# Kernel tuning notes

Hardware: AMD Instinct MI355X
Metric: run time of the kernel (lower is better)

Reference implementation:

```python
import jax, jax.numpy as jnp
import numpy as np

KERNEL = 5
STRIDE = 1
DN = ('NHWC', 'HWIO', 'NHWC')
PRIOR_VAR = 0.01


def setup_inputs() -> dict:
    key = jax.random.key(0)
    k1, k2, k3 = jax.random.split(key, 3)
    mu_in = jax.random.normal(k1, (32, 224, 224, 3), dtype=jnp.float32)
    # GlorotNormal-ish scale for a 5x5x3 -> 64 kernel
    w_mu = jax.random.normal(k2, (5, 5, 3, 64), dtype=jnp.float32) * 0.12
    # original init: uniform in [min_sigma, ini_sigma] = [-4.6, -2.25]
    w_sigma = jax.random.uniform(k3, (64,), dtype=jnp.float32, minval=-4.6, maxval=-2.25)
    return {"mu_in": mu_in, "w_mu": w_mu, "w_sigma": w_sigma}


def reference(mu_in, w_mu, w_sigma):
    # KL regularizer: broadcast of (64,) logvar against (5,5,3,64) mu, mean over all
    kl = 0.5 * jnp.mean(
        jnp.log(PRIOR_VAR) - 1.0 - w_sigma
        + jax.nn.softplus(w_sigma) / PRIOR_VAR
        + jnp.square(w_mu) / PRIOR_VAR
    )

    w_sigma_2 = jax.nn.softplus(w_sigma)  # log(1+exp(w_sigma))

    # Mean path: standard conv2d, VALID, stride 1, NHWC
    mu_out = jax.lax.conv_general_dilated(
        mu_in, w_mu, (STRIDE, STRIDE), 'VALID', dimension_numbers=DN
    )  # [B, Ho, Wo, K]

    # Variance path: per-output-location sum over the k*k*C patch of x^2 / x_dim.
    # Same math as the original extract_patches + reduce_sum, but computed as a
    # channel-summed box filter on x^2 (no im2col materialization).
    C = mu_in.shape[-1]
    x_dim = jnp.asarray(KERNEL * KERNEL * C, mu_in.dtype)
    ones_k = jnp.ones((KERNEL, KERNEL, C, 1), mu_in.dtype)
    sq = jax.lax.conv_general_dilated(
        jnp.square(mu_in), ones_k, (STRIDE, STRIDE), 'VALID', dimension_numbers=DN
    ) / x_dim  # [B, Ho, Wo, 1]

    Sigma_out = jax.nn.softplus(w_sigma_2 * sq)  # broadcast -> [B, Ho, Wo, K]
    return (mu_out, Sigma_out, kl)
```

## Files before the change

### kernel.cpp

```cpp
#include <hip/hip_runtime.h>
#include <math.h>

#define BATCH 32
#define HIN   224
#define WIN   224
#define CIN   3
#define KOUT  64
#define RK    5
#define HOUT  220
#define WOUT  220

#define TS       16
#define PATCH    20
#define NT_TILES (14 * 14 * BATCH)
#define NBLK     1024
#define NTOT ((size_t)BATCH * HOUT * WOUT * KOUT)

typedef float  v4f    __attribute__((ext_vector_type(4)));
typedef short  short8 __attribute__((ext_vector_type(8)));

#define WS_WF_FRAGS 768
#define WS_WSG_OFF  12288
#define WS_CNT_OFF  12544

__device__ __forceinline__ float exp2_hw(float x) { float r; asm("v_exp_f32 %0, %1" : "=v"(r) : "v"(x)); return r; }
__device__ __forceinline__ float log2_hw(float x) { float r; asm("v_log_f32 %0, %1" : "=v"(r) : "v"(x)); return r; }
#define LOG2E 1.44269504088896f
#define LN2   0.69314718055995f

__device__ __forceinline__ float softplus_hw(float x) {
    float t = exp2_hw(-fabsf(x) * LOG2E);
    return fmaxf(x, 0.0f) + LN2 * log2_hw(1.0f + t);
}
__device__ __forceinline__ float softplus_pos(float y) {
    return y + LN2 * log2_hw(1.0f + exp2_hw(-y * LOG2E));
}
__device__ __forceinline__ short f2bf(float x) {
    unsigned u = __float_as_uint(x);
    u = (u + 0x7FFFu + ((u >> 16) & 1u)) >> 16;
    return (short)u;
}

__global__ __launch_bounds__(256) void vdp_prep_kernel(
    const float* __restrict__ w_mu, const float* __restrict__ w_sigma,
    void* __restrict__ ws, float* __restrict__ out)
{
    __shared__ float red[4];
    short8* wf = (short8*)ws;
    float* wsg = (float*)((char*)ws + WS_WSG_OFF);
    const int t = threadIdx.x;

    if (t == 0) *(int*)((char*)ws + WS_CNT_OFF) = NBLK;

    for (int f = t; f < WS_WF_FRAGS; f += 256) {
        const int s  = f >> 8;
        const int nb = (f >> 6) & 3;
        const int l  = f & 63;
        const int ch = nb * 16 + (l & 15);
        const int h2 = l >> 4;
        short8 r;
        #pragma unroll
        for (int i = 0; i < 8; ++i) {
            const int k = s * 32 + h2 * 8 + i;
            const int kh = k >> 4, inner = k & 15;
            float v = 0.0f;
            if (inner < 15 && k < 80) {
                const int kw = inner / 3;
                const int c  = inner - kw * 3;
                v = w_mu[((kh * 5 + kw) * 3 + c) * KOUT + ch];
            }
            r[i] = f2bf(v);
        }
        wf[f] = r;
    }
    if (t < KOUT) wsg[t] = softplus_hw(w_sigma[t]);

    float s = 0.0f;
    for (int i = t; i < RK * RK * CIN * KOUT; i += 256) {
        const float v = w_mu[i];
        s = fmaf(v, v, s);
    }
    float u = s * (100.0f / 4800.0f);
    if (t < KOUT) {
        const float wsv = w_sigma[t];
        u += (-wsv + softplus_hw(wsv) * 100.0f) * (1.0f / 64.0f);
    }
    #pragma unroll
    for (int off = 32; off > 0; off >>= 1)
        u += __shfl_down(u, off, 64);
    if ((t & 63) == 0) red[t >> 6] = u;
    __syncthreads();
    if (t == 0) {
        const float U = red[0] + red[1] + red[2] + red[3];
        out[2 * NTOT] = 0.5f * (-4.6051701860f - 1.0f + U);
    }
}

__device__ __forceinline__ void stage_tile(const float* __restrict__ mu_in, int t,
                                           float* buf, int tid)
{
    const int b  = t / 196;
    const int r2 = t - b * 196;
    int ho0 = (r2 / 14) * TS; if (ho0 > HOUT - TS) ho0 = HOUT - TS;
    int wo0 = (r2 % 14) * TS; if (wo0 > WOUT - TS) wo0 = WOUT - TS;
    const float* gb = mu_in + ((size_t)b * HIN + ho0) * (WIN * CIN) + wo0 * CIN;
    #pragma unroll
    for (int it = 0; it < 2; ++it) {
        const int ci = it * 256 + (tid & ~63);
        if (ci < 320) {
            const int il = ci + (tid & 63);
            const int r  = il >> 4;
            int cc = il & 15; if (cc > 14) cc = 14;
            const float* g = gb + r * (WIN * CIN) + cc * 4;
            __builtin_amdgcn_global_load_lds(
                (const __attribute__((address_space(1))) void*)g,
                (__attribute__((address_space(3))) void*)(buf + ci * 4),
                16, 0, 0);
        }
    }
}

__global__ __launch_bounds__(256, 4) void vdp_conv_kernel(
    const float* __restrict__ mu_in, void* __restrict__ ws, float* __restrict__ out)
{
    __shared__ float s_row[2][PATCH * 64];
    __shared__ float s_ssq[PATCH][PATCH];
    __shared__ float s_sq[TS * TS];
    __shared__ int   s_next;

    const int tid  = threadIdx.x;
    const int lane = tid & 63;
    const int wid  = tid >> 6;
    const int p    = lane & 15;
    const int h2   = lane >> 4;

    int* cnt = (int*)((char*)ws + WS_CNT_OFF);

    const short8* wfg = (const short8*)ws;
    short8 wf[12];
    #pragma unroll
    for (int f = 0; f < 12; ++f) wf[f] = wfg[f * 64 + lane];
    const float* wsg_g = (const float*)((const char*)ws + WS_WSG_OFF);
    const v4f wsg_kg = *(const v4f*)(wsg_g + p * 4);

    int t = blockIdx.x;
    int cur = 0;
    stage_tile(mu_in, t, s_row[0], tid);
    asm volatile("s_waitcnt vmcnt(0)" ::: "memory");

    while (t < NT_TILES) {
        asm volatile("s_waitcnt vmcnt(24) lgkmcnt(0)" ::: "memory");
        __builtin_amdgcn_s_barrier();
        __builtin_amdgcn_sched_barrier(0);

        const float* srow = s_row[cur];

        if (tid == 0) s_next = atomicAdd(cnt, 1);

        for (int idx = tid; idx < PATCH * PATCH; idx += 256) {
            const int r = idx / PATCH;
            const int px = idx - r * PATCH;
            const float x0 = srow[r * 64 + 3 * px], x1 = srow[r * 64 + 3 * px + 1],
                        x2 = srow[r * 64 + 3 * px + 2];
            s_ssq[r][px] = fmaf(x0, x0, fmaf(x1, x1, x2 * x2));
        }
        asm volatile("s_waitcnt lgkmcnt(0)" ::: "memory");
        __builtin_amdgcn_s_barrier();

        {
            const int pr = tid >> 4, pc = tid & 15;
            float acc = 0.0f;
            #pragma unroll
            for (int kh = 0; kh < RK; ++kh)
                #pragma unroll
                for (int kw = 0; kw < RK; ++kw)
                    acc += s_ssq[pr + kh][pc + kw];
            s_sq[tid] = acc * (1.0f / 75.0f);
        }
        asm volatile("s_waitcnt lgkmcnt(0)" ::: "memory");
        __builtin_amdgcn_s_barrier();

        const int tn = s_next;
        if (tn < NT_TILES) stage_tile(mu_in, tn, s_row[cur ^ 1], tid);
        __builtin_amdgcn_sched_barrier(0);

        const int b  = t / 196;
        const int r2 = t - b * 196;
        int ho0 = (r2 / 14) * TS; if (ho0 > HOUT - TS) ho0 = HOUT - TS;
        int wo0 = (r2 % 14) * TS; if (wo0 > WOUT - TS) wo0 = WOUT - TS;

        #pragma unroll 1
        for (int j = 0; j < 4; ++j) {
            const int rt = (wid << 2) | j;
            const size_t rowbase = (((size_t)b * HOUT + ho0 + rt) * WOUT + wo0) * KOUT;

            short8 pf[3];
            #pragma unroll
            for (int s = 0; s < 3; ++s) {
                int ridx = rt + 2 * s + (h2 >> 1);
                ridx = ridx > PATCH - 1 ? PATCH - 1 : ridx;
                const float* rp = srow + ridx * 64 + 3 * p + 8 * (h2 & 1);
                union { unsigned u[4]; short8 v; } cv;
                asm("v_cvt_pk_bf16_f32 %0, %1, %2" : "=v"(cv.u[0]) : "v"(rp[0]), "v"(rp[1]));
                asm("v_cvt_pk_bf16_f32 %0, %1, %2" : "=v"(cv.u[1]) : "v"(rp[2]), "v"(rp[3]));
                asm("v_cvt_pk_bf16_f32 %0, %1, %2" : "=v"(cv.u[2]) : "v"(rp[4]), "v"(rp[5]));
                asm("v_cvt_pk_bf16_f32 %0, %1, %2" : "=v"(cv.u[3]) : "v"(rp[6]), "v"(rp[7]));
                pf[s] = cv.v;
            }

            v4f acc[4];
            #pragma unroll
            for (int nb = 0; nb < 4; ++nb) {
                v4f a = {0.0f, 0.0f, 0.0f, 0.0f};
                #pragma unroll
                for (int s = 0; s < 3; ++s)
                    a = __builtin_amdgcn_mfma_f32_16x16x32_bf16(wf[s * 4 + nb], pf[s], a, 0, 0, 0);
                acc[nb] = a;
            }

            float* mp = out + rowbase + (size_t)p * KOUT + h2 * 4;
            #pragma unroll
            for (int nb = 0; nb < 4; ++nb)
                *(v4f*)(mp + nb * 16) = acc[nb];

            float* sp = out + NTOT + rowbase + p * 4;
            #pragma unroll
            for (int pp = 0; pp < 4; ++pp) {
                const int px = (h2 << 2) | pp;
                const float sq = s_sq[(rt << 4) | px];
                v4f sg;
                sg.x = softplus_pos(wsg_kg.x * sq);
                sg.y = softplus_pos(wsg_kg.y * sq);
                sg.z = softplus_pos(wsg_kg.z * sq);
                sg.w = softplus_pos(wsg_kg.w * sq);
                *(v4f*)(sp + (size_t)px * KOUT) = sg;
            }
        }

        t = tn;
        cur ^= 1;
    }
}

extern "C" void kernel_launch(void* const* d_in, const int* in_sizes, int n_in,
                              void* d_out, int out_size, void* d_ws, size_t ws_size,
                              hipStream_t stream)
{
    (void)in_sizes; (void)n_in; (void)ws_size; (void)out_size;
    const float* mu_in   = (const float*)d_in[0];
    const float* w_mu    = (const float*)d_in[1];
    const float* w_sigma = (const float*)d_in[2];
    float* out = (float*)d_out;

    vdp_prep_kernel<<<1, 256, 0, stream>>>(w_mu, w_sigma, d_ws, out);
    vdp_conv_kernel<<<NBLK, 256, 0, stream>>>(mu_in, d_ws, out);
}
```

Baseline: 186.5 us.

## Replace 16x16 tiles with full-width two-row strips and separable box filter

Each block now processes four consecutive full-width strips of two output rows each. Blocks are assigned statically with an XCD-aware block remap, replacing the atomic work-stealing counter. Each strip stages six contiguous input rows into LDS with double buffering. The variance box filter is computed separably, with column sums first and a horizontal 5-tap sum at output time. The aim is contiguous global loads and row-contiguous output writes, plus removal of the atomic scheduling overhead. The costs are roughly twice as much staged input per output pixel and a much larger LDS footprint, which could pressure occupancy.

```diff
diff --git a/kernel.cpp b/kernel.cpp
--- a/kernel.cpp
+++ b/kernel.cpp
@@ -10,10 +10,12 @@
 #define HOUT  220
 #define WOUT  220
 
-#define TS       16
-#define PATCH    20
-#define NT_TILES (14 * 14 * BATCH)
-#define NBLK     1024
+#define STRIPS_Y  110
+#define NSTRIP    (STRIPS_Y * BATCH)
+#define NBLK      880
+#define ROWF      (WIN * CIN)
+#define SROW_FL   (6 * ROWF)
+#define SROW_CH   (SROW_FL / 4)
 #define NTOT ((size_t)BATCH * HOUT * WOUT * KOUT)
 
 typedef float  v4f    __attribute__((ext_vector_type(4)));
@@ -21,7 +23,6 @@
 
 #define WS_WF_FRAGS 768
 #define WS_WSG_OFF  12288
-#define WS_CNT_OFF  12544
 
 __device__ __forceinline__ float exp2_hw(float x) { float r; asm("v_exp_f32 %0, %1" : "=v"(r) : "v"(x)); return r; }
 __device__ __forceinline__ float log2_hw(float x) { float r; asm("v_log_f32 %0, %1" : "=v"(r) : "v"(x)); return r; }
@@ -49,8 +50,6 @@
     short8* wf = (short8*)ws;
     float* wsg = (float*)((char*)ws + WS_WSG_OFF);
     const int t = threadIdx.x;
-
-    if (t == 0) *(int*)((char*)ws + WS_CNT_OFF) = NBLK;
 
     for (int f = t; f < WS_WF_FRAGS; f += 256) {
         const int s  = f >> 8;
@@ -96,45 +95,45 @@
     }
 }
 
-__device__ __forceinline__ void stage_tile(const float* __restrict__ mu_in, int t,
-                                           float* buf, int tid)
-{
-    const int b  = t / 196;
-    const int r2 = t - b * 196;
-    int ho0 = (r2 / 14) * TS; if (ho0 > HOUT - TS) ho0 = HOUT - TS;
-    int wo0 = (r2 % 14) * TS; if (wo0 > WOUT - TS) wo0 = WOUT - TS;
-    const float* gb = mu_in + ((size_t)b * HIN + ho0) * (WIN * CIN) + wo0 * CIN;
+__device__ __forceinline__ void stage_strip(const float* __restrict__ mu_in, int t,
+                                            float* buf, int tid)
+{
+    const int b  = t / STRIPS_Y;
+    const int sy = t - b * STRIPS_Y;
+    const float* gb = mu_in + ((size_t)b * HIN + sy * 2) * ROWF;
     #pragma unroll
-    for (int it = 0; it < 2; ++it) {
+    for (int it = 0; it < 4; ++it) {
         const int ci = it * 256 + (tid & ~63);
-        if (ci < 320) {
+        if (ci < SROW_CH) {
             const int il = ci + (tid & 63);
-            const int r  = il >> 4;
-            int cc = il & 15; if (cc > 14) cc = 14;
-            const float* g = gb + r * (WIN * CIN) + cc * 4;
-            __builtin_amdgcn_global_load_lds(
-                (const __attribute__((address_space(1))) void*)g,
-                (__attribute__((address_space(3))) void*)(buf + ci * 4),
-                16, 0, 0);
+            if (il < SROW_CH) {
+                __builtin_amdgcn_global_load_lds(
+                    (const __attribute__((address_space(1))) void*)(gb + il * 4),
+                    (__attribute__((address_space(3))) void*)(buf + ci * 4),
+                    16, 0, 0);
+            }
         }
     }
 }
 
 __global__ __launch_bounds__(256, 4) void vdp_conv_kernel(
-    const float* __restrict__ mu_in, void* __restrict__ ws, float* __restrict__ out)
-{
-    __shared__ float s_row[2][PATCH * 64];
-    __shared__ float s_ssq[PATCH][PATCH];
-    __shared__ float s_sq[TS * TS];
-    __shared__ int   s_next;
+    const float* __restrict__ mu_in, const void* __restrict__ ws, float* __restrict__ out)
+{
+    __shared__ float s_row[2][SROW_FL];
+    __shared__ float s_ssq[6][224];
+    __shared__ float s_cs[2][224];
 
     const int tid  = threadIdx.x;
     const int lane = tid & 63;
     const int wid  = tid >> 6;
     const int p    = lane & 15;
     const int h2   = lane >> 4;
-
-    int* cnt = (int*)((char*)ws + WS_CNT_OFF);
+    const int rt   = wid & 1;
+    const int half = wid >> 1;
+
+    const int bid = blockIdx.x;
+    const int wg  = (bid & 7) * (NBLK / 8) + (bid >> 3);
+    const int t0  = wg * 4;
 
     const short8* wfg = (const short8*)ws;
     short8 wf[12];
@@ -143,63 +142,59 @@
     const float* wsg_g = (const float*)((const char*)ws + WS_WSG_OFF);
     const v4f wsg_kg = *(const v4f*)(wsg_g + p * 4);
 
-    int t = blockIdx.x;
+    stage_strip(mu_in, t0, s_row[0], tid);
+    __syncthreads();
+
     int cur = 0;
-    stage_tile(mu_in, t, s_row[0], tid);
-    asm volatile("s_waitcnt vmcnt(0)" ::: "memory");
-
-    while (t < NT_TILES) {
-        asm volatile("s_waitcnt vmcnt(24) lgkmcnt(0)" ::: "memory");
-        __builtin_amdgcn_s_barrier();
+    #pragma unroll 1
+    for (int k4 = 0; k4 < 4; ++k4) {
+        const int t  = t0 + k4;
+        const int b  = t / STRIPS_Y;
+        const int sy = t - b * STRIPS_Y;
+        const int r0 = sy * 2;
+
+        if (k4 < 3) stage_strip(mu_in, t + 1, s_row[cur ^ 1], tid);
         __builtin_amdgcn_sched_barrier(0);
 
         const float* srow = s_row[cur];
 
-        if (tid == 0) s_next = atomicAdd(cnt, 1);
-
-        for (int idx = tid; idx < PATCH * PATCH; idx += 256) {
-            const int r = idx / PATCH;
-            const int px = idx - r * PATCH;
-            const float x0 = srow[r * 64 + 3 * px], x1 = srow[r * 64 + 3 * px + 1],
-                        x2 = srow[r * 64 + 3 * px + 2];
-            s_ssq[r][px] = fmaf(x0, x0, fmaf(x1, x1, x2 * x2));
+        #pragma unroll
+        for (int i = 0; i < 6; ++i) {
+            const int idx = i * 256 + tid;
+            if (idx < 6 * 224) {
+                const int r = idx / 224, px = idx - r * 224;
+                const float* q = srow + r * ROWF + 3 * px;
+                s_ssq[r][px] = fmaf(q[0], q[0], fmaf(q[1], q[1], q[2] * q[2]));
+            }
         }
         asm volatile("s_waitcnt lgkmcnt(0)" ::: "memory");
         __builtin_amdgcn_s_barrier();
 
-        {
-            const int pr = tid >> 4, pc = tid & 15;
-            float acc = 0.0f;
-            #pragma unroll
-            for (int kh = 0; kh < RK; ++kh)
-                #pragma unroll
-                for (int kw = 0; kw < RK; ++kw)
-                    acc += s_ssq[pr + kh][pc + kw];
-            s_sq[tid] = acc * (1.0f / 75.0f);
+        #pragma unroll
+        for (int i = 0; i < 2; ++i) {
+            const int idx = i * 256 + tid;
+            if (idx < 2 * 224) {
+                const int rr = idx / 224, px = idx - rr * 224;
+                s_cs[rr][px] = s_ssq[rr][px] + s_ssq[rr + 1][px] + s_ssq[rr + 2][px]
+                             + s_ssq[rr + 3][px] + s_ssq[rr + 4][px];
+            }
         }
         asm volatile("s_waitcnt lgkmcnt(0)" ::: "memory");
         __builtin_amdgcn_s_barrier();
 
-        const int tn = s_next;
-        if (tn < NT_TILES) stage_tile(mu_in, tn, s_row[cur ^ 1], tid);
-        __builtin_amdgcn_sched_barrier(0);
-
-        const int b  = t / 196;
-        const int r2 = t - b * 196;
-        int ho0 = (r2 / 14) * TS; if (ho0 > HOUT - TS) ho0 = HOUT - TS;
-        int wo0 = (r2 % 14) * TS; if (wo0 > WOUT - TS) wo0 = WOUT - TS;
+        const size_t rowbase = ((size_t)b * HOUT + r0 + rt) * WOUT * KOUT;
 
         #pragma unroll 1
-        for (int j = 0; j < 4; ++j) {
-            const int rt = (wid << 2) | j;
-            const size_t rowbase = (((size_t)b * HOUT + ho0 + rt) * WOUT + wo0) * KOUT;
+        for (int g = 0; g < 7; ++g) {
+            int wo = half ? 112 + 16 * g : 16 * g;
+            if (wo > WOUT - 16) wo = WOUT - 16;
 
             short8 pf[3];
             #pragma unroll
             for (int s = 0; s < 3; ++s) {
                 int ridx = rt + 2 * s + (h2 >> 1);
-                ridx = ridx > PATCH - 1 ? PATCH - 1 : ridx;
-                const float* rp = srow + ridx * 64 + 3 * p + 8 * (h2 & 1);
+                ridx = ridx > 5 ? 5 : ridx;
+                const float* rp = srow + ridx * ROWF + 3 * (wo + p) + 8 * (h2 & 1);
                 union { unsigned u[4]; short8 v; } cv;
                 asm("v_cvt_pk_bf16_f32 %0, %1, %2" : "=v"(cv.u[0]) : "v"(rp[0]), "v"(rp[1]));
                 asm("v_cvt_pk_bf16_f32 %0, %1, %2" : "=v"(cv.u[1]) : "v"(rp[2]), "v"(rp[3]));
@@ -207,7 +202,6 @@
                 asm("v_cvt_pk_bf16_f32 %0, %1, %2" : "=v"(cv.u[3]) : "v"(rp[6]), "v"(rp[7]));
                 pf[s] = cv.v;
             }
-
             v4f acc[4];
             #pragma unroll
             for (int nb = 0; nb < 4; ++nb) {
@@ -217,17 +211,21 @@
                     a = __builtin_amdgcn_mfma_f32_16x16x32_bf16(wf[s * 4 + nb], pf[s], a, 0, 0, 0);
                 acc[nb] = a;
             }
-
-            float* mp = out + rowbase + (size_t)p * KOUT + h2 * 4;
+            float* mp = out + rowbase + (size_t)(wo + p) * KOUT + h2 * 4;
             #pragma unroll
             for (int nb = 0; nb < 4; ++nb)
                 *(v4f*)(mp + nb * 16) = acc[nb];
-
+        }
+
+        {
+            const int px0 = half * 112;
+            const int nq  = half ? 27 : 28;
             float* sp = out + NTOT + rowbase + p * 4;
-            #pragma unroll
-            for (int pp = 0; pp < 4; ++pp) {
-                const int px = (h2 << 2) | pp;
-                const float sq = s_sq[(rt << 4) | px];
+            #pragma unroll 1
+            for (int q = 0; q < nq; ++q) {
+                const int px = px0 + ((q << 2) | h2);
+                const float sq = (s_cs[rt][px] + s_cs[rt][px + 1] + s_cs[rt][px + 2]
+                                + s_cs[rt][px + 3] + s_cs[rt][px + 4]) * (1.0f / 75.0f);
                 v4f sg;
                 sg.x = softplus_pos(wsg_kg.x * sq);
                 sg.y = softplus_pos(wsg_kg.y * sq);
@@ -237,7 +235,8 @@
             }
         }
 
-        t = tn;
+        asm volatile("s_waitcnt vmcnt(48) lgkmcnt(0)" ::: "memory");
+        __builtin_amdgcn_s_barrier();
         cur ^= 1;
     }
 }
```

After: 196.4 us. 1.05x slower.

## Replace persistent atomic tile scheduler with one-block-per-tile grid launch

Applied to the files above, without the earlier changes.

Drops the persistent-kernel design, with its atomic work counter and double-buffered LDS prefetch of the next tile, in favour of a 3D grid where each block handles exactly one 16x16 output tile. The variance box-filter sum moves out of a separate LDS pass: it is computed per row in registers and broadcast with wave shuffles, so the s_sq buffer and one barrier disappear. The prep kernel is also spread over four blocks. The launch now has about six thousand blocks instead of 1024 persistent ones, which loses the overlap of tile loading with compute but removes the atomic and the loop overhead. Each block also reloads the weight fragments, which the persistent version loaded only once per block.

```diff
diff --git a/kernel.cpp b/kernel.cpp
--- a/kernel.cpp
+++ b/kernel.cpp
@@ -12,8 +12,6 @@
 
 #define TS       16
 #define PATCH    20
-#define NT_TILES (14 * 14 * BATCH)
-#define NBLK     1024
 #define NTOT ((size_t)BATCH * HOUT * WOUT * KOUT)
 
 typedef float  v4f    __attribute__((ext_vector_type(4)));
@@ -21,7 +19,6 @@
 
 #define WS_WF_FRAGS 768
 #define WS_WSG_OFF  12288
-#define WS_CNT_OFF  12544
 
 __device__ __forceinline__ float exp2_hw(float x) { float r; asm("v_exp_f32 %0, %1" : "=v"(r) : "v"(x)); return r; }
 __device__ __forceinline__ float log2_hw(float x) { float r; asm("v_log_f32 %0, %1" : "=v"(r) : "v"(x)); return r; }
@@ -49,10 +46,10 @@
     short8* wf = (short8*)ws;
     float* wsg = (float*)((char*)ws + WS_WSG_OFF);
     const int t = threadIdx.x;
-
-    if (t == 0) *(int*)((char*)ws + WS_CNT_OFF) = NBLK;
-
-    for (int f = t; f < WS_WF_FRAGS; f += 256) {
+    const int blk = blockIdx.x;
+
+    if (blk < 3) {
+        const int f = blk * 256 + t;
         const int s  = f >> 8;
         const int nb = (f >> 6) & 3;
         const int l  = f & 63;
@@ -72,7 +69,9 @@
             r[i] = f2bf(v);
         }
         wf[f] = r;
-    }
+        return;
+    }
+
     if (t < KOUT) wsg[t] = softplus_hw(w_sigma[t]);
 
     float s = 0.0f;
@@ -96,37 +95,11 @@
     }
 }
 
-__device__ __forceinline__ void stage_tile(const float* __restrict__ mu_in, int t,
-                                           float* buf, int tid)
+__global__ __launch_bounds__(256, 4) void vdp_conv_kernel(
+    const float* __restrict__ mu_in, const void* __restrict__ ws, float* __restrict__ out)
 {
-    const int b  = t / 196;
-    const int r2 = t - b * 196;
-    int ho0 = (r2 / 14) * TS; if (ho0 > HOUT - TS) ho0 = HOUT - TS;
-    int wo0 = (r2 % 14) * TS; if (wo0 > WOUT - TS) wo0 = WOUT - TS;
-    const float* gb = mu_in + ((size_t)b * HIN + ho0) * (WIN * CIN) + wo0 * CIN;
-    #pragma unroll
-    for (int it = 0; it < 2; ++it) {
-        const int ci = it * 256 + (tid & ~63);
-        if (ci < 320) {
-            const int il = ci + (tid & 63);
-            const int r  = il >> 4;
-            int cc = il & 15; if (cc > 14) cc = 14;
-            const float* g = gb + r * (WIN * CIN) + cc * 4;
-            __builtin_amdgcn_global_load_lds(
-                (const __attribute__((address_space(1))) void*)g,
-                (__attribute__((address_space(3))) void*)(buf + ci * 4),
-                16, 0, 0);
-        }
-    }
-}
-
-__global__ __launch_bounds__(256, 4) void vdp_conv_kernel(
-    const float* __restrict__ mu_in, void* __restrict__ ws, float* __restrict__ out)
-{
-    __shared__ float s_row[2][PATCH * 64];
+    __shared__ float s_row[PATCH * 64];
     __shared__ float s_ssq[PATCH][PATCH];
-    __shared__ float s_sq[TS * TS];
-    __shared__ int   s_next;
 
     const int tid  = threadIdx.x;
     const int lane = tid & 63;
@@ -134,7 +107,9 @@
     const int p    = lane & 15;
     const int h2   = lane >> 4;
 
-    int* cnt = (int*)((char*)ws + WS_CNT_OFF);
+    const int b = blockIdx.z;
+    int ho0 = blockIdx.y * TS; if (ho0 > HOUT - TS) ho0 = HOUT - TS;
+    int wo0 = blockIdx.x * TS; if (wo0 > WOUT - TS) wo0 = WOUT - TS;
 
     const short8* wfg = (const short8*)ws;
     short8 wf[12];
@@ -143,102 +118,91 @@
     const float* wsg_g = (const float*)((const char*)ws + WS_WSG_OFF);
     const v4f wsg_kg = *(const v4f*)(wsg_g + p * 4);
 
-    int t = blockIdx.x;
-    int cur = 0;
-    stage_tile(mu_in, t, s_row[0], tid);
-    asm volatile("s_waitcnt vmcnt(0)" ::: "memory");
-
-    while (t < NT_TILES) {
-        asm volatile("s_waitcnt vmcnt(24) lgkmcnt(0)" ::: "memory");
-        __builtin_amdgcn_s_barrier();
-        __builtin_amdgcn_sched_barrier(0);
-
-        const float* srow = s_row[cur];
-
-        if (tid == 0) s_next = atomicAdd(cnt, 1);
-
-        for (int idx = tid; idx < PATCH * PATCH; idx += 256) {
-            const int r = idx / PATCH;
-            const int px = idx - r * PATCH;
-            const float x0 = srow[r * 64 + 3 * px], x1 = srow[r * 64 + 3 * px + 1],
-                        x2 = srow[r * 64 + 3 * px + 2];
-            s_ssq[r][px] = fmaf(x0, x0, fmaf(x1, x1, x2 * x2));
-        }
-        asm volatile("s_waitcnt lgkmcnt(0)" ::: "memory");
-        __builtin_amdgcn_s_barrier();
-
-        {
-            const int pr = tid >> 4, pc = tid & 15;
-            float acc = 0.0f;
+    {
+        const float* gb = mu_in + ((size_t)b * HIN + ho0) * (WIN * CIN) + wo0 * CIN;
+        #pragma unroll
+        for (int it = 0; it < 2; ++it) {
+            const int ci = it * 256 + (tid & ~63);
+            if (ci < 320) {
+                const int il = ci + (tid & 63);
+                const int r  = il >> 4;
+                int cc = il & 15; if (cc > 14) cc = 14;
+                const float* g = gb + r * (WIN * CIN) + cc * 4;
+                __builtin_amdgcn_global_load_lds(
+                    (const __attribute__((address_space(1))) void*)g,
+                    (__attribute__((address_space(3))) void*)(s_row + ci * 4),
+                    16, 0, 0);
+            }
+        }
+    }
+    asm volatile("s_waitcnt vmcnt(0) lgkmcnt(0)" ::: "memory");
+    __builtin_amdgcn_s_barrier();
+
+    for (int idx = tid; idx < PATCH * PATCH; idx += 256) {
+        const int r = idx / PATCH;
+        const int px = idx - r * PATCH;
+        const float x0 = s_row[r * 64 + 3 * px], x1 = s_row[r * 64 + 3 * px + 1],
+                    x2 = s_row[r * 64 + 3 * px + 2];
+        s_ssq[r][px] = fmaf(x0, x0, fmaf(x1, x1, x2 * x2));
+    }
+    asm volatile("s_waitcnt lgkmcnt(0)" ::: "memory");
+    __builtin_amdgcn_s_barrier();
+
+    #pragma unroll 1
+    for (int j = 0; j < 4; ++j) {
+        const int rt = (wid << 2) | j;
+        const size_t rowbase = (((size_t)b * HOUT + ho0 + rt) * WOUT + wo0) * KOUT;
+
+        short8 pf[3];
+        #pragma unroll
+        for (int s = 0; s < 3; ++s) {
+            int ridx = rt + 2 * s + (h2 >> 1);
+            ridx = ridx > PATCH - 1 ? PATCH - 1 : ridx;
+            const float* rp = s_row + ridx * 64 + 3 * p + 8 * (h2 & 1);
+            union { unsigned u[4]; short8 v; } cv;
+            asm("v_cvt_pk_bf16_f32 %0, %1, %2" : "=v"(cv.u[0]) : "v"(rp[0]), "v"(rp[1]));
+            asm("v_cvt_pk_bf16_f32 %0, %1, %2" : "=v"(cv.u[1]) : "v"(rp[2]), "v"(rp[3]));
+            asm("v_cvt_pk_bf16_f32 %0, %1, %2" : "=v"(cv.u[2]) : "v"(rp[4]), "v"(rp[5]));
+            asm("v_cvt_pk_bf16_f32 %0, %1, %2" : "=v"(cv.u[3]) : "v"(rp[6]), "v"(rp[7]));
+            pf[s] = cv.v;
+        }
+
+        v4f acc[4];
+        #pragma unroll
+        for (int nb = 0; nb < 4; ++nb) {
+            v4f a = {0.0f, 0.0f, 0.0f, 0.0f};
+            #pragma unroll
+            for (int s = 0; s < 3; ++s)
+                a = __builtin_amdgcn_mfma_f32_16x16x32_bf16(wf[s * 4 + nb], pf[s], a, 0, 0, 0);
+            acc[nb] = a;
+        }
+
+        float* mp = out + rowbase + (size_t)p * KOUT + h2 * 4;
+        #pragma unroll
+        for (int nb = 0; nb < 4; ++nb)
+            *(v4f*)(mp + nb * 16) = acc[nb];
+
+        float sqv = 0.0f;
+        if (lane < 16) {
             #pragma unroll
             for (int kh = 0; kh < RK; ++kh)
                 #pragma unroll
                 for (int kw = 0; kw < RK; ++kw)
-                    acc += s_ssq[pr + kh][pc + kw];
-            s_sq[tid] = acc * (1.0f / 75.0f);
-        }
-        asm volatile("s_waitcnt lgkmcnt(0)" ::: "memory");
-        __builtin_amdgcn_s_barrier();
-
-        const int tn = s_next;
-        if (tn < NT_TILES) stage_tile(mu_in, tn, s_row[cur ^ 1], tid);
-        __builtin_amdgcn_sched_barrier(0);
-
-        const int b  = t / 196;
-        const int r2 = t - b * 196;
-        int ho0 = (r2 / 14) * TS; if (ho0 > HOUT - TS) ho0 = HOUT - TS;
-        int wo0 = (r2 % 14) * TS; if (wo0 > WOUT - TS) wo0 = WOUT - TS;
-
-        #pragma unroll 1
-        for (int j = 0; j < 4; ++j) {
-            const int rt = (wid << 2) | j;
-            const size_t rowbase = (((size_t)b * HOUT + ho0 + rt) * WOUT + wo0) * KOUT;
-
-            short8 pf[3];
-            #pragma unroll
-            for (int s = 0; s < 3; ++s) {
-                int ridx = rt + 2 * s + (h2 >> 1);
-                ridx = ridx > PATCH - 1 ? PATCH - 1 : ridx;
-                const float* rp = srow + ridx * 64 + 3 * p + 8 * (h2 & 1);
-                union { unsigned u[4]; short8 v; } cv;
-                asm("v_cvt_pk_bf16_f32 %0, %1, %2" : "=v"(cv.u[0]) : "v"(rp[0]), "v"(rp[1]));
-                asm("v_cvt_pk_bf16_f32 %0, %1, %2" : "=v"(cv.u[1]) : "v"(rp[2]), "v"(rp[3]));
-                asm("v_cvt_pk_bf16_f32 %0, %1, %2" : "=v"(cv.u[2]) : "v"(rp[4]), "v"(rp[5]));
-                asm("v_cvt_pk_bf16_f32 %0, %1, %2" : "=v"(cv.u[3]) : "v"(rp[6]), "v"(rp[7]));
-                pf[s] = cv.v;
-            }
-
-            v4f acc[4];
-            #pragma unroll
-            for (int nb = 0; nb < 4; ++nb) {
-                v4f a = {0.0f, 0.0f, 0.0f, 0.0f};
-                #pragma unroll
-                for (int s = 0; s < 3; ++s)
-                    a = __builtin_amdgcn_mfma_f32_16x16x32_bf16(wf[s * 4 + nb], pf[s], a, 0, 0, 0);
-                acc[nb] = a;
-            }
-
-            float* mp = out + rowbase + (size_t)p * KOUT + h2 * 4;
-            #pragma unroll
-            for (int nb = 0; nb < 4; ++nb)
-                *(v4f*)(mp + nb * 16) = acc[nb];
-
-            float* sp = out + NTOT + rowbase + p * 4;
-            #pragma unroll
-            for (int pp = 0; pp < 4; ++pp) {
-                const int px = (h2 << 2) | pp;
-                const float sq = s_sq[(rt << 4) | px];
-                v4f sg;
-                sg.x = softplus_pos(wsg_kg.x * sq);
-                sg.y = softplus_pos(wsg_kg.y * sq);
-                sg.z = softplus_pos(wsg_kg.z * sq);
-                sg.w = softplus_pos(wsg_kg.w * sq);
-                *(v4f*)(sp + (size_t)px * KOUT) = sg;
-            }
-        }
-
-        t = tn;
-        cur ^= 1;
+                    sqv += s_ssq[rt + kh][p + kw];
+            sqv *= (1.0f / 75.0f);
+        }
+        float* sp = out + NTOT + rowbase + p * 4;
+        #pragma unroll
+        for (int pp = 0; pp < 4; ++pp) {
+            const int px = (h2 << 2) | pp;
+            const float sq = __shfl(sqv, px, 64);
+            v4f sg;
+            sg.x = softplus_pos(wsg_kg.x * sq);
+            sg.y = softplus_pos(wsg_kg.y * sq);
+            sg.z = softplus_pos(wsg_kg.z * sq);
+            sg.w = softplus_pos(wsg_kg.w * sq);
+            *(v4f*)(sp + (size_t)px * KOUT) = sg;
+        }
     }
 }
 
@@ -252,6 +216,7 @@
     const float* w_sigma = (const float*)d_in[2];
     float* out = (float*)d_out;
 
-    vdp_prep_kernel<<<1, 256, 0, stream>>>(w_mu, w_sigma, d_ws, out);
-    vdp_conv_kernel<<<NBLK, 256, 0, stream>>>(mu_in, d_ws, out);
-}
+    vdp_prep_kernel<<<4, 256, 0, stream>>>(w_mu, w_sigma, d_ws, out);
+    dim3 grid((WOUT + TS - 1) / TS, (HOUT + TS - 1) / TS, BATCH);
+    vdp_conv_kernel<<<grid, 256, 0, stream>>>(mu_in, d_ws, out);
+}
```

Measured after the change: 172.0 us. 1.08x faster.
